# Performance work log

Measured on AMD Instinct MI355X. Metric: run time of the kernel, lower is better.

The kernel has to match this reference:

```python
import jax, jax.numpy as jnp
import numpy as np

N_NODES = 384
HEIGHT = 60
C = 128
N_LAYERS = 4
EDGE_CH = 5
EPS = 1e-5


def _create_board(base=0):
    board = np.zeros((8, 8), dtype=int)
    num = 0
    for i in range(0, 8, 2):
        for j in range(0, 8, 2):
            board[i, j] = num
            board[i, j + 1] = num + 1
            board[i + 1, j] = num + 2
            board[i + 1, j + 1] = num + 3
            num += 4
    return np.fliplr(np.rot90(board, k=2)) + base * 64


def _get_neighbors(face, i, j):
    nb = []
    if i > 0: nb.append(face[i - 1, j])
    if i < 7: nb.append(face[i + 1, j])
    if j > 0: nb.append(face[i, j - 1])
    if j < 7: nb.append(face[i, j + 1])
    return nb


def _get_boundary_neighbors(faces):
    boundary = {i: [] for i in range(N_NODES)}
    connections = [(0,'left',3,'right','same'),(0,'up',5,'down','same'),(0,'right',1,'left','same'),(0,'down',4,'up','same'),(1,'left',0,'right','same'),(1,'up',5,'right','reverse'),(1,'right',2,'left','same'),(1,'down',4,'right','same'),(2,'left',1,'right','same'),(2,'up',5,'up','reverse'),(2,'right',3,'left','same'),(2,'down',4,'down','reverse'),(3,'left',2,'right','same'),(3,'up',5,'left','same'),(3,'right',0,'left','same'),(3,'down',4,'left','reverse'),(4,'left',3,'down','reverse'),(4,'up',0,'down','same'),(4,'right',1,'down','same'),(4,'down',2,'down','reverse'),(5,'left',3,'up','same'),(5,'up',2,'up','reverse'),(5,'right',1,'up','reverse'),(5,'down',0,'up','same')]

    def coord(index, edge, reverse):
        if edge == 'left':  c = (index, 0)
        elif edge == 'right': c = (index, 7)
        elif edge == 'up':  c = (0, index)
        else:               c = (7, index)
        if reverse:
            c = (7 - index, c[1]) if edge in ('left', 'right') else (c[0], 7 - index)
        return c

    for f1, e1, f2, e2, order in connections:
        for i in range(8):
            c1 = coord(i, e1, False)
            c2 = coord(i, e2, order == 'reverse')
            boundary[faces[f1][c1]].append(faces[f2][c2])
            boundary[faces[f2][c2]].append(faces[f1][c1])
    return boundary


def _create_edge_index():
    adj = np.zeros((N_NODES, N_NODES), dtype=int)
    faces = [_create_board(base=i) for i in range(6)]
    for face in faces:
        for i in range(8):
            for j in range(8):
                idx = face[i, j]
                for nb in _get_neighbors(face, i, j):
                    adj[idx, nb] = 1
                    adj[nb, idx] = 1
    for idx, nbs in _get_boundary_neighbors(faces).items():
        for nb in nbs:
            adj[idx, nb] = 1
            adj[nb, idx] = 1
    for i in range(N_NODES):
        for j in range(i + 1, N_NODES):
            if i // 4 == j // 4:
                adj[i, j] = 1
                adj[j, i] = 1
    np.fill_diagonal(adj, 1)  # self_loop
    return np.array(np.nonzero(adj))  # (2, E), E = 3072


def setup_inputs() -> dict:
    key = jax.random.key(0)
    k_x, k_ew, k_cw = jax.random.split(key, 3)
    ei = _create_edge_index()
    # edge_attr = sin/cos of lat/lon diffs + is_same_spectral (5 features)
    rng = np.random.default_rng(0)
    lat = np.radians(rng.uniform(-90.0, 90.0, N_NODES))
    lon = np.radians(rng.uniform(0.0, 360.0, N_NODES))
    lat_d = lat[ei[0]] - lat[ei[1]]
    lon_d = lon[ei[0]] - lon[ei[1]]
    same = (ei[0] // 4 == ei[1] // 4).astype(np.float32)
    ea = np.stack([np.sin(lat_d), np.cos(lat_d), np.sin(lon_d), np.cos(lon_d), same], axis=1).astype(np.float32)
    x = jax.random.normal(k_x, (N_NODES, C, HEIGHT), dtype=jnp.float32)
    return {
        "x": x,
        "edge_attr": jnp.asarray(ea),
        "edge_w": jax.random.normal(k_ew, (N_LAYERS, C, EDGE_CH), dtype=jnp.float32) * 0.3,
        "edge_b": jnp.zeros((N_LAYERS, C), dtype=jnp.float32),
        "conv_w": jax.random.normal(k_cw, (N_LAYERS, C, 3 * C), dtype=jnp.float32) / np.float32(np.sqrt(3 * C)),
        "ln_g": jnp.ones((N_LAYERS, C, HEIGHT), dtype=jnp.float32),
        "ln_b": jnp.zeros((N_LAYERS, C, HEIGHT), dtype=jnp.float32),
        "edge_index": jnp.asarray(ei, dtype=jnp.int32),
    }


def _layer(x, edge_index, edge_attr, ew, eb, cw, g, b):
    # x: (N, C, H); edge_index: (2, E)
    src, dst = edge_index[0], edge_index[1]
    h_i = x[dst]                                 # (E, C, H) target (x_i)
    h_j = x[src]                                 # (E, C, H) source (x_j)
    e = edge_attr @ ew.T + eb                    # (E, C) edge_linear
    e = jnp.broadcast_to(e[:, :, None], h_i.shape)
    h = jnp.concatenate([h_i, h_j - h_i, e], axis=1)   # (E, 3C, H)
    h = jnp.einsum('ekh,ck->ech', h, cw)                # kernel-size-1 Conv1d
    mu = jnp.mean(h, axis=(1, 2), keepdims=True)        # LayerNorm over (C, H)
    var = jnp.mean((h - mu) ** 2, axis=(1, 2), keepdims=True)
    h = (h - mu) * jax.lax.rsqrt(var + EPS) * g + b
    h = jax.nn.relu(h)
    return jax.ops.segment_sum(h, dst, num_segments=N_NODES)  # aggr='add'


def reference(x, edge_attr, edge_w, edge_b, conv_w, ln_g, ln_b, edge_index):
    for l in range(N_LAYERS):
        x = _layer(x, edge_index, edge_attr, edge_w[l], edge_b[l], conv_w[l], ln_g[l], ln_b[l])
    return x  # (384, C, 60)
```

## Files before the change

### kernel.cpp

```cpp
#include <hip/hip_runtime.h>
#include <hip/hip_bf16.h>

#define NN 384
#define CC 128
#define HH 60
#define NEL (CC*HH)
#define NLAYERS 4

typedef _Float16 f16x4 __attribute__((ext_vector_type(4)));
typedef float f32x4 __attribute__((ext_vector_type(4)));

__device__ __forceinline__ void cvt2(float v, _Float16& hi, _Float16& lo) {
    hi = (_Float16)v; lo = (_Float16)(v - (float)hi);
}

__global__ __launch_bounds__(256) void k_setup(
    const float* __restrict__ cw, const float* __restrict__ ew, const float* __restrict__ eb,
    const float* __restrict__ lg, const float* __restrict__ lb, const int* __restrict__ ei, int E,
    float* __restrict__ M3, float* __restrict__ v3,
    _Float16* __restrict__ wfh, _Float16* __restrict__ wfl,
    float* __restrict__ gp, float* __restrict__ bp,
    int* __restrict__ off, int* __restrict__ ssrc, int* __restrict__ seid)
{
    int bid = blockIdx.x, t = threadIdx.x;
    if (bid == 0) {
        __shared__ int cnt[NN + 1];
        __shared__ int cur[NN];
        for (int i = t; i < NN + 1; i += 256) cnt[i] = 0;
        __syncthreads();
        const int* dstp = ei + E;
        for (int e = t; e < E; e += 256) atomicAdd(&cnt[dstp[e] + 1], 1);
        __syncthreads();
        if (t == 0) { int s = 0; for (int i = 0; i <= NN; i++) { s += cnt[i]; cnt[i] = s; } }
        __syncthreads();
        for (int i = t; i < NN + 1; i += 256) off[i] = cnt[i];
        for (int i = t; i < NN; i += 256) cur[i] = cnt[i];
        __syncthreads();
        for (int e = t; e < E; e += 256) {
            int d = dstp[e];
            int p = atomicAdd(&cur[d], 1);
            ssrc[p] = ei[e];
            seid[p] = e;
        }
    } else if (bid < 5) {
        if (t < CC) {
            int l = bid - 1, c = t;
            const float* wrow = cw + (l * CC + c) * (3 * CC) + 2 * CC;
            const float* ewl = ew + l * CC * 5;
            const float* ebl = eb + l * CC;
            float m0 = 0, m1 = 0, m2 = 0, m3 = 0, m4 = 0, v = 0;
            for (int k = 0; k < CC; k++) {
                float wv = wrow[k];
                const float* e5 = ewl + k * 5;
                m0 = fmaf(wv, e5[0], m0); m1 = fmaf(wv, e5[1], m1); m2 = fmaf(wv, e5[2], m2);
                m3 = fmaf(wv, e5[3], m3); m4 = fmaf(wv, e5[4], m4);
                v  = fmaf(wv, ebl[k], v);
            }
            float* mo = M3 + (l * CC + c) * 5;
            mo[0] = m0; mo[1] = m1; mo[2] = m2; mo[3] = m3; mo[4] = m4;
            v3[l * CC + c] = v;
        }
    } else if (bid < 21) {
        int wid = ((bid - 5) << 2) + (t >> 6);
        int lane = t & 63;
        int l = wid >> 4;
        const float* cwl = cw + l * CC * 3 * CC;
        int r = ((wid & 15) << 4) + (lane & 15);
#pragma unroll
        for (int kt = 0; kt < 8; kt++) {
#pragma unroll
            for (int j = 0; j < 4; j++) {
                int k = (kt << 4) + ((lane >> 4) << 2) + j;
                float wv;
                if (r < 128) wv = cwl[r * 384 + k] - cwl[r * 384 + 128 + k];
                else         wv = cwl[(r - 128) * 384 + 128 + k];
                _Float16 hi, lo; cvt2(wv, hi, lo);
                int idx = (wid * 8 + kt) * 256 + lane * 4 + j;
                wfh[idx] = hi; wfl[idx] = lo;
            }
        }
    } else if (bid < 141) {
        int gidx = ((bid - 21) << 8) + t;
        int l = gidx / NEL, q = gidx - l * NEL;
        int c = q & 127, h = q >> 7;
        gp[gidx] = lg[l * NEL + c * HH + h];
        bp[gidx] = lb[l * NEL + c * HH + h];
    }
}

__device__ __forceinline__ void mm_core(char* XhB, char* XlB,
                                        const _Float16* __restrict__ wfhL,
                                        const _Float16* __restrict__ wflL,
                                        float* __restrict__ Dout, int n, int w, int lane)
{
    f16x4 whv[4][8], wlv[4][8];
#pragma unroll
    for (int nt = 0; nt < 4; nt++)
#pragma unroll
        for (int kt = 0; kt < 8; kt++) {
            int idx = (((((w << 2) + nt) << 3) + kt) << 8) + (lane << 2);
            whv[nt][kt] = *(const f16x4*)(wfhL + idx);
            wlv[nt][kt] = *(const f16x4*)(wflL + idx);
        }
    f32x4 acc[4][4];
#pragma unroll
    for (int mt = 0; mt < 4; mt++)
#pragma unroll
        for (int nt = 0; nt < 4; nt++) acc[mt][nt] = (f32x4){0.f, 0.f, 0.f, 0.f};

#pragma unroll
    for (int ks = 0; ks < 8; ks++) {
        f16x4 ah[4], al[4];
#pragma unroll
        for (int mt = 0; mt < 4; mt++) {
            int h = (mt << 4) + (lane & 15);
            int o = (h << 8) + (((ks << 5) + ((lane >> 4) << 3)) ^ ((h & 7) << 4));
            ah[mt] = *(const f16x4*)(XhB + o);
            al[mt] = *(const f16x4*)(XlB + o);
        }
#pragma unroll
        for (int mt = 0; mt < 4; mt++)
#pragma unroll
            for (int nt = 0; nt < 4; nt++) {
                acc[mt][nt] = __builtin_amdgcn_mfma_f32_16x16x16f16(ah[mt], whv[nt][ks], acc[mt][nt], 0, 0, 0);
                acc[mt][nt] = __builtin_amdgcn_mfma_f32_16x16x16f16(al[mt], whv[nt][ks], acc[mt][nt], 0, 0, 0);
                acc[mt][nt] = __builtin_amdgcn_mfma_f32_16x16x16f16(ah[mt], wlv[nt][ks], acc[mt][nt], 0, 0, 0);
            }
    }
    int rb = w << 6;
#pragma unroll
    for (int mt = 0; mt < 4; mt++) {
        int hb = (mt << 4) + ((lane >> 4) << 2);
#pragma unroll
        for (int nt = 0; nt < 4; nt++) {
            int r = rb + (nt << 4) + (lane & 15);
#pragma unroll
            for (int reg = 0; reg < 4; reg++) {
                int h = hb + reg;
                if (h < HH) Dout[(n * HH + h) * 256 + r] = acc[mt][nt][reg];
            }
        }
    }
}

__global__ __launch_bounds__(256, 2) void k_mm0(const float* __restrict__ x,
                                                const _Float16* __restrict__ wfhL,
                                                const _Float16* __restrict__ wflL,
                                                float* __restrict__ Dout)
{
    __shared__ __align__(16) char smem[33024];
    char* XhB = smem;
    char* XlB = smem + 16384;
    int n = blockIdx.x, t = threadIdx.x;
    int w = t >> 6, lane = t & 63;

    const float* xn = x + n * NEL;
    for (int p = t; p < 3840; p += 256) {
        int q = p << 1;
        int c = q & 127, h = q >> 7;
        float v0 = xn[c * HH + h], v1 = xn[(c + 1) * HH + h];
        _Float16 h0, l0, h1, l1; cvt2(v0, h0, l0); cvt2(v1, h1, l1);
        int o = (h << 8) + ((c << 1) ^ ((h & 7) << 4));
        union { _Float16 f[2]; unsigned u; } ph, pl;
        ph.f[0] = h0; ph.f[1] = h1; pl.f[0] = l0; pl.f[1] = l1;
        *(unsigned*)(XhB + o) = ph.u;
        *(unsigned*)(XlB + o) = pl.u;
    }
    if (t < 64) {
        int h = 60 + (t >> 4), ch = t & 15;
        int o = (h << 8) + ((ch << 4) ^ ((h & 7) << 4));
        *(uint4*)(XhB + o) = make_uint4(0, 0, 0, 0);
        *(uint4*)(XlB + o) = make_uint4(0, 0, 0, 0);
    }
    __syncthreads();
    mm_core(XhB, XlB, wfhL, wflL, Dout, n, w, lane);
}

template<bool LAST>
__global__ __launch_bounds__(256, 2) void k_fused(
    const float* __restrict__ Din, const float* __restrict__ ea,
    const float* __restrict__ M3l, const float* __restrict__ v3l,
    const float* __restrict__ gpl, const float* __restrict__ bpl,
    const int* __restrict__ off, const int* __restrict__ ssrc, const int* __restrict__ seid,
    const _Float16* __restrict__ wfhL, const _Float16* __restrict__ wflL,
    float* __restrict__ Dout)
{
    __shared__ __align__(16) char smem[33024];
    int d = blockIdx.x, t = threadIdx.x;
    int w = t >> 6, lane = t & 63;
    float* c3all = (float*)smem;
    float* red   = c3all + 2048;

    int j0 = off[d], j1 = off[d + 1], cnt = j1 - j0;

    for (int idx = t; idx < (cnt << 7); idx += 256) {
        int j = idx >> 7, c = idx & 127;
        int eid = seid[j0 + j];
        const float* eap = ea + eid * 5;
        const float* m = M3l + c * 5;
        c3all[idx] = v3l[c] + m[0]*eap[0] + m[1]*eap[1] + m[2]*eap[2] + m[3]*eap[3] + m[4]*eap[4];
    }

    float2 areg[15], greg[15], breg[15], accv[15], bv[15], bvn[15];
    const float2* D2 = (const float2*)Din;
    const float2* g2 = (const float2*)gpl;
    const float2* b2 = (const float2*)bpl;
#pragma unroll
    for (int i = 0; i < 15; i++) {
        int p = t + (i << 8);
        areg[i] = D2[(d * HH + (p >> 6)) * 128 + (p & 63)];
        greg[i] = g2[p]; breg[i] = b2[p];
        accv[i] = make_float2(0.f, 0.f);
    }
    {
        int s = ssrc[j0];
#pragma unroll
        for (int i = 0; i < 15; i++) {
            int p = t + (i << 8);
            bv[i] = D2[(s * HH + (p >> 6)) * 128 + 64 + (p & 63)];
        }
    }
    __syncthreads();

    for (int j = 0; j < cnt; j++) {
        if (j + 1 < cnt) {
            int s = ssrc[j0 + j + 1];
#pragma unroll
            for (int i = 0; i < 15; i++) {
                int p = t + (i << 8);
                bvn[i] = D2[(s * HH + (p >> 6)) * 128 + 64 + (p & 63)];
            }
        }
        float2 cc = ((const float2*)c3all)[(j << 6) + (t & 63)];
        float sum = 0.f, sq = 0.f;
#pragma unroll
        for (int i = 0; i < 15; i++) {
            float vx = areg[i].x + bv[i].x + cc.x;
            float vy = areg[i].y + bv[i].y + cc.y;
            sum += vx + vy;
            sq = fmaf(vx, vx, fmaf(vy, vy, sq));
        }
#pragma unroll
        for (int o = 32; o; o >>= 1) { sum += __shfl_xor(sum, o); sq += __shfl_xor(sq, o); }
        int jb = j & 1;
        if ((t & 63) == 0) { red[jb * 8 + (t >> 6) * 2] = sum; red[jb * 8 + (t >> 6) * 2 + 1] = sq; }
        asm volatile("s_waitcnt lgkmcnt(0)" ::: "memory");
        __builtin_amdgcn_s_barrier();
        float fs = red[jb*8+0] + red[jb*8+2] + red[jb*8+4] + red[jb*8+6];
        float fq = red[jb*8+1] + red[jb*8+3] + red[jb*8+5] + red[jb*8+7];
        float mu = fs * (1.0f / NEL);
        float var = fq * (1.0f / NEL) - mu * mu;
        float rs = rsqrtf(var + 1e-5f);
#pragma unroll
        for (int i = 0; i < 15; i++) {
            float vx = areg[i].x + bv[i].x + cc.x;
            float vy = areg[i].y + bv[i].y + cc.y;
            float nx = (vx - mu) * rs * greg[i].x + breg[i].x;
            float ny = (vy - mu) * rs * greg[i].y + breg[i].y;
            accv[i].x += fmaxf(nx, 0.f);
            accv[i].y += fmaxf(ny, 0.f);
            bv[i] = bvn[i];
        }
    }

    if (LAST) {
#pragma unroll
        for (int i = 0; i < 15; i++) {
            int p = t + (i << 8);
            int h = p >> 6, c = (p & 63) << 1;
            Dout[d * NEL + c * HH + h] = accv[i].x;
            Dout[d * NEL + (c + 1) * HH + h] = accv[i].y;
        }
    } else {
        __syncthreads();
        char* XhB = smem;
        char* XlB = smem + 16384;
#pragma unroll
        for (int i = 0; i < 15; i++) {
            int p = t + (i << 8);
            int h = p >> 6;
            int cb = (p & 63) << 2;
            int o = (h << 8) + (cb ^ ((h & 7) << 4));
            _Float16 h0, l0, h1, l1;
            cvt2(accv[i].x, h0, l0); cvt2(accv[i].y, h1, l1);
            union { _Float16 f[2]; unsigned u; } ph, pl;
            ph.f[0] = h0; ph.f[1] = h1; pl.f[0] = l0; pl.f[1] = l1;
            *(unsigned*)(XhB + o) = ph.u;
            *(unsigned*)(XlB + o) = pl.u;
        }
        if (t < 64) {
            int h = 60 + (t >> 4), ch = t & 15;
            int o = (h << 8) + ((ch << 4) ^ ((h & 7) << 4));
            *(uint4*)(XhB + o) = make_uint4(0, 0, 0, 0);
            *(uint4*)(XlB + o) = make_uint4(0, 0, 0, 0);
        }
        __syncthreads();
        mm_core(XhB, XlB, wfhL, wflL, Dout, d, w, lane);
    }
}

extern "C" void kernel_launch(void* const* d_in, const int* in_sizes, int n_in,
                              void* d_out, int out_size, void* d_ws, size_t ws_size,
                              hipStream_t stream) {
    const float* x  = (const float*)d_in[0];
    const float* ea = (const float*)d_in[1];
    const float* ew = (const float*)d_in[2];
    const float* eb = (const float*)d_in[3];
    const float* cw = (const float*)d_in[4];
    const float* lg = (const float*)d_in[5];
    const float* lb = (const float*)d_in[6];
    const int*   ei = (const int*)d_in[7];
    int E = in_sizes[7] / 2;
    float* out = (float*)d_out;

    float* wsf = (float*)d_ws;
    float* D0 = wsf;
    float* D1 = D0 + NN * HH * 256;
    float* gp = D1 + NN * HH * 256;
    float* bp = gp + NLAYERS * NEL;
    float* M3 = bp + NLAYERS * NEL;
    float* v3 = M3 + NLAYERS * 640;
    _Float16* wfh = (_Float16*)(v3 + NLAYERS * 128);
    _Float16* wfl = wfh + NLAYERS * 32768;
    int* off  = (int*)(wfl + NLAYERS * 32768);
    int* ssrc = off + (NN + 1);
    int* seid = ssrc + E;

    k_setup<<<141, 256, 0, stream>>>(cw, ew, eb, lg, lb, ei, E,
                                     M3, v3, wfh, wfl, gp, bp, off, ssrc, seid);
    k_mm0<<<NN, 256, 0, stream>>>(x, wfh, wfl, D0);

    k_fused<false><<<NN, 256, 0, stream>>>(D0, ea, M3 + 0 * 640, v3 + 0 * 128,
                                           gp + 0 * NEL, bp + 0 * NEL, off, ssrc, seid,
                                           wfh + 1 * 32768, wfl + 1 * 32768, D1);
    k_fused<false><<<NN, 256, 0, stream>>>(D1, ea, M3 + 1 * 640, v3 + 1 * 128,
                                           gp + 1 * NEL, bp + 1 * NEL, off, ssrc, seid,
                                           wfh + 2 * 32768, wfl + 2 * 32768, D0);
    k_fused<false><<<NN, 256, 0, stream>>>(D0, ea, M3 + 2 * 640, v3 + 2 * 128,
                                           gp + 2 * NEL, bp + 2 * NEL, off, ssrc, seid,
                                           wfh + 3 * 32768, wfl + 3 * 32768, D1);
    k_fused<true><<<NN, 256, 0, stream>>>(D1, ea, M3 + 3 * 640, v3 + 3 * 128,
                                          gp + 3 * NEL, bp + 3 * NEL, off, ssrc, seid,
                                          wfh, wfl, out);
}
```

Measured before the change: 220.0 us.

## Merge all layer kernels into one persistent kernel with grid-wide barriers

Replaces the six separate launches (setup, initial matmul, four fused layers) with a single persistent kernel of 384 blocks. Global atomic-counter barriers separate the phases, and a memset resets the counters before launch. This removes per-launch overhead and the gaps between kernels, but it relies on all 384 blocks being co-resident (2 blocks per CU is assumed) and adds spin-wait barrier latency.

```diff
diff --git a/kernel.cpp b/kernel.cpp
--- a/kernel.cpp
+++ b/kernel.cpp
@@ -14,18 +14,93 @@
     hi = (_Float16)v; lo = (_Float16)(v - (float)hi);
 }
 
-__global__ __launch_bounds__(256) void k_setup(
-    const float* __restrict__ cw, const float* __restrict__ ew, const float* __restrict__ eb,
-    const float* __restrict__ lg, const float* __restrict__ lb, const int* __restrict__ ei, int E,
+__device__ __forceinline__ void gbar(int* bar, int idx) {
+    __syncthreads();
+    if (threadIdx.x == 0) {
+        __threadfence();
+        atomicAdd(&bar[idx], 1);
+        while (__hip_atomic_load(&bar[idx], __ATOMIC_RELAXED, __HIP_MEMORY_SCOPE_AGENT) < NN)
+            __builtin_amdgcn_s_sleep(8);
+        __threadfence();
+    }
+    __syncthreads();
+}
+
+__device__ __forceinline__ void mm_core(char* XhB, char* XlB,
+                                        const _Float16* __restrict__ wfhL,
+                                        const _Float16* __restrict__ wflL,
+                                        float* __restrict__ Dout, int n, int w, int lane)
+{
+    f16x4 whv[4][8], wlv[4][8];
+#pragma unroll
+    for (int nt = 0; nt < 4; nt++)
+#pragma unroll
+        for (int kt = 0; kt < 8; kt++) {
+            int idx = (((((w << 2) + nt) << 3) + kt) << 8) + (lane << 2);
+            whv[nt][kt] = *(const f16x4*)(wfhL + idx);
+            wlv[nt][kt] = *(const f16x4*)(wflL + idx);
+        }
+    f32x4 acc[4][4];
+#pragma unroll
+    for (int mt = 0; mt < 4; mt++)
+#pragma unroll
+        for (int nt = 0; nt < 4; nt++) acc[mt][nt] = (f32x4){0.f, 0.f, 0.f, 0.f};
+
+#pragma unroll
+    for (int ks = 0; ks < 8; ks++) {
+        f16x4 ah[4], al[4];
+#pragma unroll
+        for (int mt = 0; mt < 4; mt++) {
+            int h = (mt << 4) + (lane & 15);
+            int o = (h << 8) + (((ks << 5) + ((lane >> 4) << 3)) ^ ((h & 7) << 4));
+            ah[mt] = *(const f16x4*)(XhB + o);
+            al[mt] = *(const f16x4*)(XlB + o);
+        }
+#pragma unroll
+        for (int mt = 0; mt < 4; mt++)
+#pragma unroll
+            for (int nt = 0; nt < 4; nt++) {
+                acc[mt][nt] = __builtin_amdgcn_mfma_f32_16x16x16f16(ah[mt], whv[nt][ks], acc[mt][nt], 0, 0, 0);
+                acc[mt][nt] = __builtin_amdgcn_mfma_f32_16x16x16f16(al[mt], whv[nt][ks], acc[mt][nt], 0, 0, 0);
+                acc[mt][nt] = __builtin_amdgcn_mfma_f32_16x16x16f16(ah[mt], wlv[nt][ks], acc[mt][nt], 0, 0, 0);
+            }
+    }
+    int rb = w << 6;
+#pragma unroll
+    for (int mt = 0; mt < 4; mt++) {
+        int hb = (mt << 4) + ((lane >> 4) << 2);
+#pragma unroll
+        for (int nt = 0; nt < 4; nt++) {
+            int r = rb + (nt << 4) + (lane & 15);
+#pragma unroll
+            for (int reg = 0; reg < 4; reg++) {
+                int h = hb + reg;
+                if (h < HH) Dout[(n * HH + h) * 256 + r] = acc[mt][nt][reg];
+            }
+        }
+    }
+}
+
+__global__ __launch_bounds__(256, 2) void mega(
+    const float* __restrict__ x, const float* __restrict__ ea,
+    const float* __restrict__ ew, const float* __restrict__ eb,
+    const float* __restrict__ cw, const float* __restrict__ lg,
+    const float* __restrict__ lb, const int* __restrict__ ei, int E,
+    float* __restrict__ out,
+    float* __restrict__ D0, float* __restrict__ D1,
+    float* __restrict__ gp, float* __restrict__ bp,
     float* __restrict__ M3, float* __restrict__ v3,
     _Float16* __restrict__ wfh, _Float16* __restrict__ wfl,
-    float* __restrict__ gp, float* __restrict__ bp,
-    int* __restrict__ off, int* __restrict__ ssrc, int* __restrict__ seid)
+    int* __restrict__ off, int* __restrict__ ssrc, int* __restrict__ seid,
+    int* __restrict__ bar)
 {
-    int bid = blockIdx.x, t = threadIdx.x;
+    __shared__ __align__(16) char smem[33024];
+    const int bid = blockIdx.x, t = threadIdx.x;
+    const int w = t >> 6, lane = t & 63;
+
     if (bid == 0) {
-        __shared__ int cnt[NN + 1];
-        __shared__ int cur[NN];
+        int* cnt = (int*)smem;
+        int* cur = cnt + NN + 1;
         for (int i = t; i < NN + 1; i += 256) cnt[i] = 0;
         __syncthreads();
         const int* dstp = ei + E;
@@ -61,8 +136,7 @@
             v3[l * CC + c] = v;
         }
     } else if (bid < 21) {
-        int wid = ((bid - 5) << 2) + (t >> 6);
-        int lane = t & 63;
+        int wid = ((bid - 5) << 2) + w;
         int l = wid >> 4;
         const float* cwl = cw + l * CC * 3 * CC;
         int r = ((wid & 15) << 4) + (lane & 15);
@@ -86,203 +160,18 @@
         gp[gidx] = lg[l * NEL + c * HH + h];
         bp[gidx] = lb[l * NEL + c * HH + h];
     }
-}
-
-__device__ __forceinline__ void mm_core(char* XhB, char* XlB,
-                                        const _Float16* __restrict__ wfhL,
-                                        const _Float16* __restrict__ wflL,
-                                        float* __restrict__ Dout, int n, int w, int lane)
-{
-    f16x4 whv[4][8], wlv[4][8];
-#pragma unroll
-    for (int nt = 0; nt < 4; nt++)
-#pragma unroll
-        for (int kt = 0; kt < 8; kt++) {
-            int idx = (((((w << 2) + nt) << 3) + kt) << 8) + (lane << 2);
-            whv[nt][kt] = *(const f16x4*)(wfhL + idx);
-            wlv[nt][kt] = *(const f16x4*)(wflL + idx);
-        }
-    f32x4 acc[4][4];
-#pragma unroll
-    for (int mt = 0; mt < 4; mt++)
-#pragma unroll
-        for (int nt = 0; nt < 4; nt++) acc[mt][nt] = (f32x4){0.f, 0.f, 0.f, 0.f};
-
-#pragma unroll
-    for (int ks = 0; ks < 8; ks++) {
-        f16x4 ah[4], al[4];
-#pragma unroll
-        for (int mt = 0; mt < 4; mt++) {
-            int h = (mt << 4) + (lane & 15);
-            int o = (h << 8) + (((ks << 5) + ((lane >> 4) << 3)) ^ ((h & 7) << 4));
-            ah[mt] = *(const f16x4*)(XhB + o);
-            al[mt] = *(const f16x4*)(XlB + o);
-        }
-#pragma unroll
-        for (int mt = 0; mt < 4; mt++)
-#pragma unroll
-            for (int nt = 0; nt < 4; nt++) {
-                acc[mt][nt] = __builtin_amdgcn_mfma_f32_16x16x16f16(ah[mt], whv[nt][ks], acc[mt][nt], 0, 0, 0);
-                acc[mt][nt] = __builtin_amdgcn_mfma_f32_16x16x16f16(al[mt], whv[nt][ks], acc[mt][nt], 0, 0, 0);
-                acc[mt][nt] = __builtin_amdgcn_mfma_f32_16x16x16f16(ah[mt], wlv[nt][ks], acc[mt][nt], 0, 0, 0);
-            }
-    }
-    int rb = w << 6;
-#pragma unroll
-    for (int mt = 0; mt < 4; mt++) {
-        int hb = (mt << 4) + ((lane >> 4) << 2);
-#pragma unroll
-        for (int nt = 0; nt < 4; nt++) {
-            int r = rb + (nt << 4) + (lane & 15);
-#pragma unroll
-            for (int reg = 0; reg < 4; reg++) {
-                int h = hb + reg;
-                if (h < HH) Dout[(n * HH + h) * 256 + r] = acc[mt][nt][reg];
-            }
-        }
-    }
-}
-
-__global__ __launch_bounds__(256, 2) void k_mm0(const float* __restrict__ x,
-                                                const _Float16* __restrict__ wfhL,
-                                                const _Float16* __restrict__ wflL,
-                                                float* __restrict__ Dout)
-{
-    __shared__ __align__(16) char smem[33024];
-    char* XhB = smem;
-    char* XlB = smem + 16384;
-    int n = blockIdx.x, t = threadIdx.x;
-    int w = t >> 6, lane = t & 63;
-
-    const float* xn = x + n * NEL;
-    for (int p = t; p < 3840; p += 256) {
-        int q = p << 1;
-        int c = q & 127, h = q >> 7;
-        float v0 = xn[c * HH + h], v1 = xn[(c + 1) * HH + h];
-        _Float16 h0, l0, h1, l1; cvt2(v0, h0, l0); cvt2(v1, h1, l1);
-        int o = (h << 8) + ((c << 1) ^ ((h & 7) << 4));
-        union { _Float16 f[2]; unsigned u; } ph, pl;
-        ph.f[0] = h0; ph.f[1] = h1; pl.f[0] = l0; pl.f[1] = l1;
-        *(unsigned*)(XhB + o) = ph.u;
-        *(unsigned*)(XlB + o) = pl.u;
-    }
-    if (t < 64) {
-        int h = 60 + (t >> 4), ch = t & 15;
-        int o = (h << 8) + ((ch << 4) ^ ((h & 7) << 4));
-        *(uint4*)(XhB + o) = make_uint4(0, 0, 0, 0);
-        *(uint4*)(XlB + o) = make_uint4(0, 0, 0, 0);
-    }
-    __syncthreads();
-    mm_core(XhB, XlB, wfhL, wflL, Dout, n, w, lane);
-}
-
-template<bool LAST>
-__global__ __launch_bounds__(256, 2) void k_fused(
-    const float* __restrict__ Din, const float* __restrict__ ea,
-    const float* __restrict__ M3l, const float* __restrict__ v3l,
-    const float* __restrict__ gpl, const float* __restrict__ bpl,
-    const int* __restrict__ off, const int* __restrict__ ssrc, const int* __restrict__ seid,
-    const _Float16* __restrict__ wfhL, const _Float16* __restrict__ wflL,
-    float* __restrict__ Dout)
-{
-    __shared__ __align__(16) char smem[33024];
-    int d = blockIdx.x, t = threadIdx.x;
-    int w = t >> 6, lane = t & 63;
-    float* c3all = (float*)smem;
-    float* red   = c3all + 2048;
-
-    int j0 = off[d], j1 = off[d + 1], cnt = j1 - j0;
-
-    for (int idx = t; idx < (cnt << 7); idx += 256) {
-        int j = idx >> 7, c = idx & 127;
-        int eid = seid[j0 + j];
-        const float* eap = ea + eid * 5;
-        const float* m = M3l + c * 5;
-        c3all[idx] = v3l[c] + m[0]*eap[0] + m[1]*eap[1] + m[2]*eap[2] + m[3]*eap[3] + m[4]*eap[4];
-    }
-
-    float2 areg[15], greg[15], breg[15], accv[15], bv[15], bvn[15];
-    const float2* D2 = (const float2*)Din;
-    const float2* g2 = (const float2*)gpl;
-    const float2* b2 = (const float2*)bpl;
-#pragma unroll
-    for (int i = 0; i < 15; i++) {
-        int p = t + (i << 8);
-        areg[i] = D2[(d * HH + (p >> 6)) * 128 + (p & 63)];
-        greg[i] = g2[p]; breg[i] = b2[p];
-        accv[i] = make_float2(0.f, 0.f);
-    }
+    gbar(bar, 0);
+
     {
-        int s = ssrc[j0];
-#pragma unroll
-        for (int i = 0; i < 15; i++) {
-            int p = t + (i << 8);
-            bv[i] = D2[(s * HH + (p >> 6)) * 128 + 64 + (p & 63)];
-        }
-    }
-    __syncthreads();
-
-    for (int j = 0; j < cnt; j++) {
-        if (j + 1 < cnt) {
-            int s = ssrc[j0 + j + 1];
-#pragma unroll
-            for (int i = 0; i < 15; i++) {
-                int p = t + (i << 8);
-                bvn[i] = D2[(s * HH + (p >> 6)) * 128 + 64 + (p & 63)];
-            }
-        }
-        float2 cc = ((const float2*)c3all)[(j << 6) + (t & 63)];
-        float sum = 0.f, sq = 0.f;
-#pragma unroll
-        for (int i = 0; i < 15; i++) {
-            float vx = areg[i].x + bv[i].x + cc.x;
-            float vy = areg[i].y + bv[i].y + cc.y;
-            sum += vx + vy;
-            sq = fmaf(vx, vx, fmaf(vy, vy, sq));
-        }
-#pragma unroll
-        for (int o = 32; o; o >>= 1) { sum += __shfl_xor(sum, o); sq += __shfl_xor(sq, o); }
-        int jb = j & 1;
-        if ((t & 63) == 0) { red[jb * 8 + (t >> 6) * 2] = sum; red[jb * 8 + (t >> 6) * 2 + 1] = sq; }
-        asm volatile("s_waitcnt lgkmcnt(0)" ::: "memory");
-        __builtin_amdgcn_s_barrier();
-        float fs = red[jb*8+0] + red[jb*8+2] + red[jb*8+4] + red[jb*8+6];
-        float fq = red[jb*8+1] + red[jb*8+3] + red[jb*8+5] + red[jb*8+7];
-        float mu = fs * (1.0f / NEL);
-        float var = fq * (1.0f / NEL) - mu * mu;
-        float rs = rsqrtf(var + 1e-5f);
-#pragma unroll
-        for (int i = 0; i < 15; i++) {
-            float vx = areg[i].x + bv[i].x + cc.x;
-            float vy = areg[i].y + bv[i].y + cc.y;
-            float nx = (vx - mu) * rs * greg[i].x + breg[i].x;
-            float ny = (vy - mu) * rs * greg[i].y + breg[i].y;
-            accv[i].x += fmaxf(nx, 0.f);
-            accv[i].y += fmaxf(ny, 0.f);
-            bv[i] = bvn[i];
-        }
-    }
-
-    if (LAST) {
-#pragma unroll
-        for (int i = 0; i < 15; i++) {
-            int p = t + (i << 8);
-            int h = p >> 6, c = (p & 63) << 1;
-            Dout[d * NEL + c * HH + h] = accv[i].x;
-            Dout[d * NEL + (c + 1) * HH + h] = accv[i].y;
-        }
-    } else {
-        __syncthreads();
         char* XhB = smem;
         char* XlB = smem + 16384;
-#pragma unroll
-        for (int i = 0; i < 15; i++) {
-            int p = t + (i << 8);
-            int h = p >> 6;
-            int cb = (p & 63) << 2;
-            int o = (h << 8) + (cb ^ ((h & 7) << 4));
-            _Float16 h0, l0, h1, l1;
-            cvt2(accv[i].x, h0, l0); cvt2(accv[i].y, h1, l1);
+        const float* xn = x + bid * NEL;
+        for (int p = t; p < 3840; p += 256) {
+            int q = p << 1;
+            int c = q & 127, h = q >> 7;
+            float v0 = xn[c * HH + h], v1 = xn[(c + 1) * HH + h];
+            _Float16 h0, l0, h1, l1; cvt2(v0, h0, l0); cvt2(v1, h1, l1);
+            int o = (h << 8) + ((c << 1) ^ ((h & 7) << 4));
             union { _Float16 f[2]; unsigned u; } ph, pl;
             ph.f[0] = h0; ph.f[1] = h1; pl.f[0] = l0; pl.f[1] = l1;
             *(unsigned*)(XhB + o) = ph.u;
@@ -295,7 +184,129 @@
             *(uint4*)(XlB + o) = make_uint4(0, 0, 0, 0);
         }
         __syncthreads();
-        mm_core(XhB, XlB, wfhL, wflL, Dout, d, w, lane);
+        mm_core(XhB, XlB, wfh, wfl, D0, bid, w, lane);
+    }
+    gbar(bar, 1);
+
+    const int d = bid;
+    const int j0 = off[d], j1 = off[d + 1], cnt = j1 - j0;
+
+    for (int l = 0; l < NLAYERS; l++) {
+        const float* Din = (l & 1) ? D1 : D0;
+        float* Dnext     = (l & 1) ? D0 : D1;
+        const float* M3l = M3 + l * 640;
+        const float* v3l = v3 + l * 128;
+        const float* gpl = gp + l * NEL;
+        const float* bpl = bp + l * NEL;
+
+        float* c3all = (float*)smem;
+        float* red   = c3all + 2048;
+
+        for (int idx = t; idx < (cnt << 7); idx += 256) {
+            int j = idx >> 7, c = idx & 127;
+            int eid = seid[j0 + j];
+            const float* eap = ea + eid * 5;
+            const float* m = M3l + c * 5;
+            c3all[idx] = v3l[c] + m[0]*eap[0] + m[1]*eap[1] + m[2]*eap[2] + m[3]*eap[3] + m[4]*eap[4];
+        }
+
+        float2 areg[15], greg[15], breg[15], accv[15], bv[15], bvn[15];
+        const float2* D2 = (const float2*)Din;
+        const float2* g2 = (const float2*)gpl;
+        const float2* b2 = (const float2*)bpl;
+#pragma unroll
+        for (int i = 0; i < 15; i++) {
+            int p = t + (i << 8);
+            areg[i] = D2[(d * HH + (p >> 6)) * 128 + (p & 63)];
+            greg[i] = g2[p]; breg[i] = b2[p];
+            accv[i] = make_float2(0.f, 0.f);
+        }
+        {
+            int s = ssrc[j0];
+#pragma unroll
+            for (int i = 0; i < 15; i++) {
+                int p = t + (i << 8);
+                bv[i] = D2[(s * HH + (p >> 6)) * 128 + 64 + (p & 63)];
+            }
+        }
+        __syncthreads();
+
+        for (int j = 0; j < cnt; j++) {
+            if (j + 1 < cnt) {
+                int s = ssrc[j0 + j + 1];
+#pragma unroll
+                for (int i = 0; i < 15; i++) {
+                    int p = t + (i << 8);
+                    bvn[i] = D2[(s * HH + (p >> 6)) * 128 + 64 + (p & 63)];
+                }
+            }
+            float2 cc = ((const float2*)c3all)[(j << 6) + (t & 63)];
+            float sum = 0.f, sq = 0.f;
+#pragma unroll
+            for (int i = 0; i < 15; i++) {
+                float vx = areg[i].x + bv[i].x + cc.x;
+                float vy = areg[i].y + bv[i].y + cc.y;
+                sum += vx + vy;
+                sq = fmaf(vx, vx, fmaf(vy, vy, sq));
+            }
+#pragma unroll
+            for (int o = 32; o; o >>= 1) { sum += __shfl_xor(sum, o); sq += __shfl_xor(sq, o); }
+            int jb = j & 1;
+            if ((t & 63) == 0) { red[jb * 8 + (t >> 6) * 2] = sum; red[jb * 8 + (t >> 6) * 2 + 1] = sq; }
+            asm volatile("s_waitcnt lgkmcnt(0)" ::: "memory");
+            __builtin_amdgcn_s_barrier();
+            float fs = red[jb*8+0] + red[jb*8+2] + red[jb*8+4] + red[jb*8+6];
+            float fq = red[jb*8+1] + red[jb*8+3] + red[jb*8+5] + red[jb*8+7];
+            float mu = fs * (1.0f / NEL);
+            float var = fq * (1.0f / NEL) - mu * mu;
+            float rs = rsqrtf(var + 1e-5f);
+#pragma unroll
+            for (int i = 0; i < 15; i++) {
+                float vx = areg[i].x + bv[i].x + cc.x;
+                float vy = areg[i].y + bv[i].y + cc.y;
+                float nx = (vx - mu) * rs * greg[i].x + breg[i].x;
+                float ny = (vy - mu) * rs * greg[i].y + breg[i].y;
+                accv[i].x += fmaxf(nx, 0.f);
+                accv[i].y += fmaxf(ny, 0.f);
+                bv[i] = bvn[i];
+            }
+        }
+
+        if (l == NLAYERS - 1) {
+#pragma unroll
+            for (int i = 0; i < 15; i++) {
+                int p = t + (i << 8);
+                int h = p >> 6, c = (p & 63) << 1;
+                out[d * NEL + c * HH + h] = accv[i].x;
+                out[d * NEL + (c + 1) * HH + h] = accv[i].y;
+            }
+        } else {
+            __syncthreads();
+            char* XhB = smem;
+            char* XlB = smem + 16384;
+#pragma unroll
+            for (int i = 0; i < 15; i++) {
+                int p = t + (i << 8);
+                int h = p >> 6;
+                int cb = (p & 63) << 2;
+                int o = (h << 8) + (cb ^ ((h & 7) << 4));
+                _Float16 h0, l0, h1, l1;
+                cvt2(accv[i].x, h0, l0); cvt2(accv[i].y, h1, l1);
+                union { _Float16 f[2]; unsigned u; } ph, pl;
+                ph.f[0] = h0; ph.f[1] = h1; pl.f[0] = l0; pl.f[1] = l1;
+                *(unsigned*)(XhB + o) = ph.u;
+                *(unsigned*)(XlB + o) = pl.u;
+            }
+            if (t < 64) {
+                int h = 60 + (t >> 4), ch = t & 15;
+                int o = (h << 8) + ((ch << 4) ^ ((h & 7) << 4));
+                *(uint4*)(XhB + o) = make_uint4(0, 0, 0, 0);
+                *(uint4*)(XlB + o) = make_uint4(0, 0, 0, 0);
+            }
+            __syncthreads();
+            mm_core(XhB, XlB, wfh + (l + 1) * 32768, wfl + (l + 1) * 32768, Dnext, d, w, lane);
+            gbar(bar, 2 + l);
+        }
     }
 }
 
@@ -325,21 +336,11 @@
     int* off  = (int*)(wfl + NLAYERS * 32768);
     int* ssrc = off + (NN + 1);
     int* seid = ssrc + E;
-
-    k_setup<<<141, 256, 0, stream>>>(cw, ew, eb, lg, lb, ei, E,
-                                     M3, v3, wfh, wfl, gp, bp, off, ssrc, seid);
-    k_mm0<<<NN, 256, 0, stream>>>(x, wfh, wfl, D0);
-
-    k_fused<false><<<NN, 256, 0, stream>>>(D0, ea, M3 + 0 * 640, v3 + 0 * 128,
-                                           gp + 0 * NEL, bp + 0 * NEL, off, ssrc, seid,
-                                           wfh + 1 * 32768, wfl + 1 * 32768, D1);
-    k_fused<false><<<NN, 256, 0, stream>>>(D1, ea, M3 + 1 * 640, v3 + 1 * 128,
-                                           gp + 1 * NEL, bp + 1 * NEL, off, ssrc, seid,
-                                           wfh + 2 * 32768, wfl + 2 * 32768, D0);
-    k_fused<false><<<NN, 256, 0, stream>>>(D0, ea, M3 + 2 * 640, v3 + 2 * 128,
-                                           gp + 2 * NEL, bp + 2 * NEL, off, ssrc, seid,
-                                           wfh + 3 * 32768, wfl + 3 * 32768, D1);
-    k_fused<true><<<NN, 256, 0, stream>>>(D1, ea, M3 + 3 * 640, v3 + 3 * 128,
-                                          gp + 3 * NEL, bp + 3 * NEL, off, ssrc, seid,
-                                          wfh, wfl, out);
-}
+    int* bar  = seid + E;
+
+    hipMemsetAsync(bar, 0, 8 * sizeof(int), stream);
+
+    mega<<<NN, 256, 0, stream>>>(x, ea, ew, eb, cw, lg, lb, ei, E, out,
+                                 D0, D1, gp, bp, M3, v3, wfh, wfl,
+                                 off, ssrc, seid, bar);
+}
```

Result: slower. 496.0 us (+125.4%).

## Split interleaved A/B projection buffers, remap block-to-node order, cut weight registers

Applied to the files above, without the earlier changes.

The per-node projection output is stored in two separate contiguous arrays (A for the target half, B for the source half) instead of one interleaved 256-wide row. Each gathered source read then covers one contiguous block of memory. Blocks are remapped with a strided node permutation, likely to spread work or improve cache locality across XCDs. Low-half weights are now loaded per k-step instead of being held in registers for the whole loop, and launch bounds move to 3 blocks per SM to raise occupancy. The costs are extra weight reloads from global or cache and possible register spills under the tighter bound.

```diff
diff --git a/kernel.cpp b/kernel.cpp
--- a/kernel.cpp
+++ b/kernel.cpp
@@ -13,6 +13,7 @@
 __device__ __forceinline__ void cvt2(float v, _Float16& hi, _Float16& lo) {
     hi = (_Float16)v; lo = (_Float16)(v - (float)hi);
 }
+__device__ __forceinline__ int nmap(int bid) { return ((bid & 7) * 48) + (bid >> 3); }
 
 __global__ __launch_bounds__(256) void k_setup(
     const float* __restrict__ cw, const float* __restrict__ ew, const float* __restrict__ eb,
@@ -91,17 +92,16 @@
 __device__ __forceinline__ void mm_core(char* XhB, char* XlB,
                                         const _Float16* __restrict__ wfhL,
                                         const _Float16* __restrict__ wflL,
-                                        float* __restrict__ Dout, int n, int w, int lane)
+                                        float* __restrict__ Aout, float* __restrict__ Bout,
+                                        int n, int w, int lane)
 {
-    f16x4 whv[4][8], wlv[4][8];
+    f16x4 whv[4][8];
 #pragma unroll
     for (int nt = 0; nt < 4; nt++)
 #pragma unroll
-        for (int kt = 0; kt < 8; kt++) {
-            int idx = (((((w << 2) + nt) << 3) + kt) << 8) + (lane << 2);
-            whv[nt][kt] = *(const f16x4*)(wfhL + idx);
-            wlv[nt][kt] = *(const f16x4*)(wflL + idx);
-        }
+        for (int kt = 0; kt < 8; kt++)
+            whv[nt][kt] = *(const f16x4*)(wfhL + (((((w << 2) + nt) << 3) + kt) << 8) + (lane << 2));
+
     f32x4 acc[4][4];
 #pragma unroll
     for (int mt = 0; mt < 4; mt++)
@@ -110,6 +110,10 @@
 
 #pragma unroll
     for (int ks = 0; ks < 8; ks++) {
+        f16x4 wlv[4];
+#pragma unroll
+        for (int nt = 0; nt < 4; nt++)
+            wlv[nt] = *(const f16x4*)(wflL + (((((w << 2) + nt) << 3) + ks) << 8) + (lane << 2));
         f16x4 ah[4], al[4];
 #pragma unroll
         for (int mt = 0; mt < 4; mt++) {
@@ -124,34 +128,34 @@
             for (int nt = 0; nt < 4; nt++) {
                 acc[mt][nt] = __builtin_amdgcn_mfma_f32_16x16x16f16(ah[mt], whv[nt][ks], acc[mt][nt], 0, 0, 0);
                 acc[mt][nt] = __builtin_amdgcn_mfma_f32_16x16x16f16(al[mt], whv[nt][ks], acc[mt][nt], 0, 0, 0);
-                acc[mt][nt] = __builtin_amdgcn_mfma_f32_16x16x16f16(ah[mt], wlv[nt][ks], acc[mt][nt], 0, 0, 0);
+                acc[mt][nt] = __builtin_amdgcn_mfma_f32_16x16x16f16(ah[mt], wlv[nt], acc[mt][nt], 0, 0, 0);
             }
     }
-    int rb = w << 6;
+    float* Out = ((w < 2) ? Aout : Bout) + n * NEL + ((w & 1) << 6);
 #pragma unroll
     for (int mt = 0; mt < 4; mt++) {
         int hb = (mt << 4) + ((lane >> 4) << 2);
 #pragma unroll
         for (int nt = 0; nt < 4; nt++) {
-            int r = rb + (nt << 4) + (lane & 15);
+            int rl = (nt << 4) + (lane & 15);
 #pragma unroll
             for (int reg = 0; reg < 4; reg++) {
                 int h = hb + reg;
-                if (h < HH) Dout[(n * HH + h) * 256 + r] = acc[mt][nt][reg];
+                if (h < HH) Out[h * 128 + rl] = acc[mt][nt][reg];
             }
         }
     }
 }
 
-__global__ __launch_bounds__(256, 2) void k_mm0(const float* __restrict__ x,
+__global__ __launch_bounds__(256, 3) void k_mm0(const float* __restrict__ x,
                                                 const _Float16* __restrict__ wfhL,
                                                 const _Float16* __restrict__ wflL,
-                                                float* __restrict__ Dout)
+                                                float* __restrict__ Aout, float* __restrict__ Bout)
 {
     __shared__ __align__(16) char smem[33024];
     char* XhB = smem;
     char* XlB = smem + 16384;
-    int n = blockIdx.x, t = threadIdx.x;
+    int n = nmap(blockIdx.x), t = threadIdx.x;
     int w = t >> 6, lane = t & 63;
 
     const float* xn = x + n * NEL;
@@ -173,20 +177,21 @@
         *(uint4*)(XlB + o) = make_uint4(0, 0, 0, 0);
     }
     __syncthreads();
-    mm_core(XhB, XlB, wfhL, wflL, Dout, n, w, lane);
+    mm_core(XhB, XlB, wfhL, wflL, Aout, Bout, n, w, lane);
 }
 
 template<bool LAST>
-__global__ __launch_bounds__(256, 2) void k_fused(
-    const float* __restrict__ Din, const float* __restrict__ ea,
+__global__ __launch_bounds__(256, 3) void k_fused(
+    const float* __restrict__ Ain, const float* __restrict__ Bin,
+    const float* __restrict__ ea,
     const float* __restrict__ M3l, const float* __restrict__ v3l,
     const float* __restrict__ gpl, const float* __restrict__ bpl,
     const int* __restrict__ off, const int* __restrict__ ssrc, const int* __restrict__ seid,
     const _Float16* __restrict__ wfhL, const _Float16* __restrict__ wflL,
-    float* __restrict__ Dout)
+    float* __restrict__ Aout, float* __restrict__ Bout)
 {
     __shared__ __align__(16) char smem[33024];
-    int d = blockIdx.x, t = threadIdx.x;
+    int d = nmap(blockIdx.x), t = threadIdx.x;
     int w = t >> 6, lane = t & 63;
     float* c3all = (float*)smem;
     float* red   = c3all + 2048;
@@ -202,34 +207,27 @@
     }
 
     float2 areg[15], greg[15], breg[15], accv[15], bv[15], bvn[15];
-    const float2* D2 = (const float2*)Din;
+    const float2* A2 = (const float2*)(Ain + d * NEL);
     const float2* g2 = (const float2*)gpl;
     const float2* b2 = (const float2*)bpl;
 #pragma unroll
     for (int i = 0; i < 15; i++) {
         int p = t + (i << 8);
-        areg[i] = D2[(d * HH + (p >> 6)) * 128 + (p & 63)];
-        greg[i] = g2[p]; breg[i] = b2[p];
+        areg[i] = A2[p]; greg[i] = g2[p]; breg[i] = b2[p];
         accv[i] = make_float2(0.f, 0.f);
     }
     {
-        int s = ssrc[j0];
-#pragma unroll
-        for (int i = 0; i < 15; i++) {
-            int p = t + (i << 8);
-            bv[i] = D2[(s * HH + (p >> 6)) * 128 + 64 + (p & 63)];
-        }
+        const float2* B2 = (const float2*)(Bin + ssrc[j0] * NEL);
+#pragma unroll
+        for (int i = 0; i < 15; i++) bv[i] = B2[t + (i << 8)];
     }
     __syncthreads();
 
     for (int j = 0; j < cnt; j++) {
         if (j + 1 < cnt) {
-            int s = ssrc[j0 + j + 1];
-#pragma unroll
-            for (int i = 0; i < 15; i++) {
-                int p = t + (i << 8);
-                bvn[i] = D2[(s * HH + (p >> 6)) * 128 + 64 + (p & 63)];
-            }
+            const float2* B2 = (const float2*)(Bin + ssrc[j0 + j + 1] * NEL);
+#pragma unroll
+            for (int i = 0; i < 15; i++) bvn[i] = B2[t + (i << 8)];
         }
         float2 cc = ((const float2*)c3all)[(j << 6) + (t & 63)];
         float sum = 0.f, sq = 0.f;
@@ -268,8 +266,8 @@
         for (int i = 0; i < 15; i++) {
             int p = t + (i << 8);
             int h = p >> 6, c = (p & 63) << 1;
-            Dout[d * NEL + c * HH + h] = accv[i].x;
-            Dout[d * NEL + (c + 1) * HH + h] = accv[i].y;
+            Aout[d * NEL + c * HH + h] = accv[i].x;
+            Aout[d * NEL + (c + 1) * HH + h] = accv[i].y;
         }
     } else {
         __syncthreads();
@@ -295,7 +293,7 @@
             *(uint4*)(XlB + o) = make_uint4(0, 0, 0, 0);
         }
         __syncthreads();
-        mm_core(XhB, XlB, wfhL, wflL, Dout, d, w, lane);
+        mm_core(XhB, XlB, wfhL, wflL, Aout, Bout, d, w, lane);
     }
 }
 
@@ -314,9 +312,11 @@
     float* out = (float*)d_out;
 
     float* wsf = (float*)d_ws;
-    float* D0 = wsf;
-    float* D1 = D0 + NN * HH * 256;
-    float* gp = D1 + NN * HH * 256;
+    float* A0 = wsf;
+    float* B0 = A0 + NN * NEL;
+    float* A1 = B0 + NN * NEL;
+    float* B1 = A1 + NN * NEL;
+    float* gp = B1 + NN * NEL;
     float* bp = gp + NLAYERS * NEL;
     float* M3 = bp + NLAYERS * NEL;
     float* v3 = M3 + NLAYERS * 640;
@@ -328,18 +328,18 @@
 
     k_setup<<<141, 256, 0, stream>>>(cw, ew, eb, lg, lb, ei, E,
                                      M3, v3, wfh, wfl, gp, bp, off, ssrc, seid);
-    k_mm0<<<NN, 256, 0, stream>>>(x, wfh, wfl, D0);
-
-    k_fused<false><<<NN, 256, 0, stream>>>(D0, ea, M3 + 0 * 640, v3 + 0 * 128,
+    k_mm0<<<NN, 256, 0, stream>>>(x, wfh, wfl, A0, B0);
+
+    k_fused<false><<<NN, 256, 0, stream>>>(A0, B0, ea, M3 + 0 * 640, v3 + 0 * 128,
                                            gp + 0 * NEL, bp + 0 * NEL, off, ssrc, seid,
-                                           wfh + 1 * 32768, wfl + 1 * 32768, D1);
-    k_fused<false><<<NN, 256, 0, stream>>>(D1, ea, M3 + 1 * 640, v3 + 1 * 128,
+                                           wfh + 1 * 32768, wfl + 1 * 32768, A1, B1);
+    k_fused<false><<<NN, 256, 0, stream>>>(A1, B1, ea, M3 + 1 * 640, v3 + 1 * 128,
                                            gp + 1 * NEL, bp + 1 * NEL, off, ssrc, seid,
-                                           wfh + 2 * 32768, wfl + 2 * 32768, D0);
-    k_fused<false><<<NN, 256, 0, stream>>>(D0, ea, M3 + 2 * 640, v3 + 2 * 128,
+                                           wfh + 2 * 32768, wfl + 2 * 32768, A0, B0);
+    k_fused<false><<<NN, 256, 0, stream>>>(A0, B0, ea, M3 + 2 * 640, v3 + 2 * 128,
                                            gp + 2 * NEL, bp + 2 * NEL, off, ssrc, seid,
-                                           wfh + 3 * 32768, wfl + 3 * 32768, D1);
-    k_fused<true><<<NN, 256, 0, stream>>>(D1, ea, M3 + 3 * 640, v3 + 3 * 128,
+                                           wfh + 3 * 32768, wfl + 3 * 32768, A1, B1);
+    k_fused<true><<<NN, 256, 0, stream>>>(A1, B1, ea, M3 + 3 * 640, v3 + 3 * 128,
                                           gp + 3 * NEL, bp + 3 * NEL, off, ssrc, seid,
-                                          wfh, wfl, out);
-}
+                                          wfh, wfl, out, out);
+}
```

After: 352.9 us. +60.4%, slower.
